# Optimization experiments

Hardware: AMD Instinct MI355X
Metric: run time of the kernel (lower is better)

The kernel has to match this reference:

```python
import jax, jax.numpy as jnp
import numpy as np

K = 10
EPS = 1e-5
SLOPE = 0.01
B, FIN, FOUT, N = 16, 128, 128, 2048


def _bn(x, g, b, axes):
    # training-mode batchnorm over given axes (channel dim is axis 1)
    m = jnp.mean(x, axis=axes, keepdims=True)
    v = jnp.var(x, axis=axes, keepdims=True)
    sh = [1] * x.ndim
    sh[1] = -1
    return (x - m) * jax.lax.rsqrt(v + EPS) * g.reshape(sh) + b.reshape(sh)


def _lrelu(x):
    return jnp.where(x >= 0, x, SLOPE * x)


def _conv1x1(x, W, b):
    return jnp.einsum('bcnk,oc->bonk', x, W) + b[None, :, None, None]


def _forward(x, pc, Wf, bf, gf, betaf, Wx, bx, gx, betax, Wa1, ba1, ga1, beta_a1, Wa2, ba2, ga2, beta_a2, Wi, bi, gi, beta_i, W2, b2, g2, beta2):
    Bsz, Fin, Npts = x.shape
    k = K
    # --- kNN graph build: pairwise sq-dist via bmm, full sort, drop self ---
    sq = jnp.sum(x * x, axis=1)  # [B,N]
    dist = -2.0 * jnp.einsum('bdn,bdm->bnm', x, x) + sq[:, :, None] + sq[:, None, :]
    idx = jnp.argsort(dist, axis=2)[:, :, 1:k + 1]  # [B,N,k]
    gather = jax.vmap(lambda f, i: f[:, i])  # [C,N],[N,k] -> [C,N,k]
    nbr = gather(x, idx)
    nbr_xyz = gather(pc, idx)
    e_fea = jnp.concatenate([jnp.broadcast_to(x[..., None], (Bsz, Fin, Npts, k)), nbr - x[..., None]], axis=1)   # [B,2Fin,N,k]
    e_xyz = jnp.concatenate([jnp.broadcast_to(pc[..., None], (Bsz, 3, Npts, k)), nbr_xyz - pc[..., None]], axis=1)  # [B,6,N,k]
    # --- bilateral attention weights ---
    w = _lrelu(_bn(_conv1x1(e_fea, Wf, bf), gf, betaf, (0, 2, 3))) * _lrelu(_bn(_conv1x1(e_xyz, Wx, bx), gx, betax, (0, 2, 3)))
    w = _lrelu(_bn(_conv1x1(w, Wa1, ba1), ga1, beta_a1, (0, 2, 3)))
    w = _lrelu(_bn(_conv1x1(w, Wa2, ba2), ga2, beta_a2, (0, 2, 3)))
    w = jax.nn.softmax(w, axis=-1)  # [B,2Fin,N,k]
    # --- interpolation conv over neighbour axis (kernel [1, k//2+1]) ---
    inte = jax.lax.conv_general_dilated(e_fea, Wi, (1, 1), 'VALID', dimension_numbers=('NCHW', 'OIHW', 'NCHW')) + bi[None, :, None, None]
    inte = _lrelu(_bn(inte, gi, beta_i, (0, 2, 3)))  # [B,4Fin,N,k-k//2]
    inte = jnp.transpose(inte, (0, 2, 1, 3)).reshape(Bsz, Npts, 2 * Fin, k)  # channel-pair interleave, same layout as torch .view
    inte = jnp.transpose(inte, (0, 2, 1, 3)) * w  # [B,2Fin,N,k]
    merge = jnp.concatenate([e_fea, inte], axis=3)  # [B,2Fin,N,2k]
    # conv2: kernel [1,2k] spans full width -> width-1 output, as einsum
    out = jnp.einsum('bcnw,ocw->bon', merge, W2[:, :, 0, :]) + b2[None, :, None]  # [B,2Fout,N]
    out = jnp.maximum(_bn(out, g2, beta2, (0, 2)), 0.0)
    Fout = out.shape[1] // 2
    return out.reshape(Bsz, Fout, 2 * Npts)


def setup_inputs() -> dict:
    ks = jax.random.split(jax.random.key(0), 10)
    s = 0.05
    return {
        'x': jax.random.normal(ks[0], (B, FIN, N), jnp.float32),
        'pc': jax.random.normal(ks[1], (B, 3, N), jnp.float32),
        'Wf': jax.random.normal(ks[2], (16, 2 * FIN), jnp.float32) * s,
        'bf': jnp.zeros((16,), jnp.float32), 'gf': jnp.ones((16,), jnp.float32), 'betaf': jnp.zeros((16,), jnp.float32),
        'Wx': jax.random.normal(ks[3], (16, 6), jnp.float32) * s,
        'bx': jnp.zeros((16,), jnp.float32), 'gx': jnp.ones((16,), jnp.float32), 'betax': jnp.zeros((16,), jnp.float32),
        'Wa1': jax.random.normal(ks[4], (64, 16), jnp.float32) * s,
        'ba1': jnp.zeros((64,), jnp.float32), 'ga1': jnp.ones((64,), jnp.float32), 'beta_a1': jnp.zeros((64,), jnp.float32),
        'Wa2': jax.random.normal(ks[5], (2 * FIN, 64), jnp.float32) * s,
        'ba2': jnp.zeros((2 * FIN,), jnp.float32), 'ga2': jnp.ones((2 * FIN,), jnp.float32), 'beta_a2': jnp.zeros((2 * FIN,), jnp.float32),
        'Wi': jax.random.normal(ks[6], (4 * FIN, 2 * FIN, 1, K // 2 + 1), jnp.float32) * s,
        'bi': jnp.zeros((4 * FIN,), jnp.float32), 'gi': jnp.ones((4 * FIN,), jnp.float32), 'beta_i': jnp.zeros((4 * FIN,), jnp.float32),
        'W2': jax.random.normal(ks[7], (2 * FOUT, 2 * FIN, 1, 2 * K), jnp.float32) * s,
        'b2': jnp.zeros((2 * FOUT,), jnp.float32), 'g2': jnp.ones((2 * FOUT,), jnp.float32), 'beta2': jnp.zeros((2 * FOUT,), jnp.float32),
    }


def reference(x, pc, Wf, bf, gf, betaf, Wx, bx, gx, betax, Wa1, ba1, ga1, beta_a1, Wa2, ba2, ga2, beta_a2, Wi, bi, gi, beta_i, W2, b2, g2, beta2):
    return _forward(x, pc, Wf, bf, gf, betaf, Wx, bx, gx, betax, Wa1, ba1, ga1, beta_a1, Wa2, ba2, ga2, beta_a2, Wi, bi, gi, beta_i, W2, b2, g2, beta2)
```

## Files before the change

kernel.cpp:

```cpp
#include <hip/hip_runtime.h>
#include <hip/hip_bf16.h>
#include <cstdio>
#include <cstddef>

#define B_    16
#define FIN_  128
#define N_    2048
#define K_    10
#define EPS_  1e-5f
#define SLOPE_ 0.01f

typedef float f32x4 __attribute__((ext_vector_type(4)));
typedef short s16x8 __attribute__((ext_vector_type(8)));
typedef short s16x4 __attribute__((ext_vector_type(4)));

constexpr int SUM_F=0,   SS_F=16,   SUM_X=32,  SS_X=48;
constexpr int SUM_A1=64, SS_A1=128, SUM_A2=192,SS_A2=448;
constexpr int SUM_I=704, SS_I=1216, SUM_O=1728,SS_O=1984;
constexpr int SCALE_F=2240, SHIFT_F=2256, SCALE_X=2272, SHIFT_X=2288;
constexpr int SCALE_A1=2304, SHIFT_A1=2368, SCALE_A2=2432, SHIFT_A2=2688;
constexpr int SCALE_I=2944, SHIFT_I=3456, SCALE_O=3968, SHIFT_O=4224;
constexpr int STATS_TOTAL=4480;
constexpr int AUX_TOTAL = 64 + 4096;

constexpr int KW2_ = 3968;
constexpr int CHUNK_ = 8192;

__device__ __forceinline__ float lrelu(float v){ return v >= 0.f ? v : SLOPE_*v; }
__device__ __forceinline__ float wave_sum(float v){
  #pragma unroll
  for (int o = 32; o > 0; o >>= 1) v += __shfl_down(v, o, 64);
  return v;
}
__device__ __forceinline__ unsigned short f2bf(float f){
  __hip_bfloat16 h = __float2bfloat16(f);
  return *reinterpret_cast<unsigned short*>(&h);
}
__device__ __forceinline__ float bf2f(unsigned short u){
  __hip_bfloat16 h = *reinterpret_cast<__hip_bfloat16*>(&u);
  return __bfloat162float(h);
}

__global__ void k_zero(float* s, float* aux){
  for (int i = threadIdx.x; i < STATS_TOTAL; i += 256) s[i] = 0.f;
  for (int i = threadIdx.x; i < AUX_TOTAL; i += 256) aux[i] = 0.f;
}

__global__ __launch_bounds__(256) void k_xt(const float* __restrict__ x, float* __restrict__ xT){
  __shared__ float t[32][33];
  const int b = blockIdx.z;
  const int c0 = blockIdx.x*32, n0 = blockIdx.y*32;
  const int tx = threadIdx.x & 31, ty = threadIdx.x >> 5;
  #pragma unroll
  for (int s = 0; s < 32; s += 8)
    t[ty+s][tx] = x[((size_t)b*FIN_ + c0+ty+s)*N_ + n0 + tx];
  __syncthreads();
  #pragma unroll
  for (int s = 0; s < 32; s += 8)
    xT[((size_t)b*N_ + n0+ty+s)*FIN_ + c0 + tx] = t[tx][ty+s];
}

__global__ __launch_bounds__(256) void k_sq(const float* __restrict__ x, float* __restrict__ sq){
  int id = blockIdx.x*256 + threadIdx.x;
  int b = id >> 11, n = id & (N_-1);
  const float* xb = x + (size_t)b*FIN_*N_ + n;
  float part[16];
  #pragma unroll
  for (int p = 0; p < 16; ++p){
    float a = 0.f;
    #pragma unroll
    for (int q = 0; q < 8; ++q){
      float v = xb[(size_t)(p + 16*q)*N_];
      a = __fmaf_rn(v, v, a);
    }
    part[p] = a;
  }
  #pragma unroll
  for (int off = 8; off > 0; off >>= 1){
    #pragma unroll
    for (int l = 0; l < off; ++l)
      part[l] = __fadd_rn(part[l], part[l+off]);
  }
  sq[id] = part[0];
}

__global__ __launch_bounds__(256, 2) void k_knn(const float* __restrict__ x, const float* __restrict__ sq,
                                                int* __restrict__ idx){
  __shared__ __align__(16) char smem[61440];
  float* xi = (float*)smem;
  const int b = blockIdx.y, i0 = blockIdx.x*64;
  const float* xb = x + (size_t)b*FIN_*N_;
  for (int t = threadIdx.x; t < FIN_*64; t += 256){
    int c = t >> 6, ii = t & 63;
    xi[t] = xb[(size_t)c*N_ + i0 + ii];
  }
  __syncthreads();
  const int ty = threadIdx.x >> 4;
  const int tx = threadIdx.x & 15;
  const int ibase = ty*4;
  const f32x4 sqi = *(const f32x4*)&sq[b*N_ + i0 + ibase];
  float bd[4][10]; int bi[4][10];
  #pragma unroll
  for (int ii=0;ii<4;++ii)
    #pragma unroll
    for (int s=0;s<10;++s){ bd[ii][s] = 1e30f; bi[ii][s] = -1; }

  for (int j0 = 0; j0 < N_; j0 += 64){
    const int jb = j0 + tx*4;
    const float* xjp = xb + jb;
    f32x4 acc[4] = {};
    #pragma unroll 8
    for (int c = 0; c < FIN_; ++c){
      const f32x4 a  = *(const f32x4*)&xi[c*64 + ibase];
      const f32x4 bb = *(const f32x4*)&xjp[(size_t)c*N_];
      #pragma unroll
      for (int ii=0;ii<4;++ii){
        #pragma unroll
        for (int m=0;m<4;++m)
          acc[ii][m] = __fmaf_rn(a[ii], bb[m], acc[ii][m]);
      }
    }
    const f32x4 sqj = *(const f32x4*)&sq[b*N_ + jb];
    #pragma unroll
    for (int ii=0;ii<4;++ii){
      const int i = i0 + ibase + ii;
      #pragma unroll
      for (int m=0;m<4;++m){
        int j = jb + m;
        float d = __fadd_rn(__fadd_rn(__fmul_rn(-2.f, acc[ii][m]), sqi[ii]), sqj[m]);
        if (j == i) d = 1e30f;
        if (d < bd[ii][9]){
          bd[ii][9] = d; bi[ii][9] = j;
          #pragma unroll
          for (int s = 9; s > 0; --s){
            if (bd[ii][s] < bd[ii][s-1]){
              float td = bd[ii][s]; bd[ii][s] = bd[ii][s-1]; bd[ii][s-1] = td;
              int ti = bi[ii][s]; bi[ii][s] = bi[ii][s-1]; bi[ii][s-1] = ti;
            }
          }
        }
      }
    }
  }

  __syncthreads();
  float* dbuf = (float*)smem;
  unsigned short* ibuf = (unsigned short*)(smem + 40960);
  #pragma unroll
  for (int ii=0;ii<4;++ii)
    #pragma unroll
    for (int s=0;s<10;++s){
      dbuf[(tx*10+s)*64 + ibase+ii] = bd[ii][s];
      ibuf[(tx*10+s)*64 + ibase+ii] = (unsigned short)bi[ii][s];
    }
  __syncthreads();
  if (threadIdx.x < 64){
    const int rr = threadIdx.x;
    int p[16];
    #pragma unroll
    for (int qq=0;qq<16;++qq) p[qq]=0;
    int* op = idx + ((size_t)b*N_ + i0 + rr)*K_;
    for (int s = 0; s < K_; ++s){
      float dm = 1e38f; int im = 0x7fffffff; int qm = 0;
      #pragma unroll
      for (int qq = 0; qq < 16; ++qq){
        int pq = p[qq];
        float d  = (pq < 10) ? dbuf[(qq*10+pq)*64 + rr] : 1e38f;
        int   jd = (pq < 10) ? (int)ibuf[(qq*10+pq)*64 + rr] : 0x7fffffff;
        bool take = (d < dm) || (d == dm && jd < im);
        if (take){ dm = d; im = jd; qm = qq; }
      }
      #pragma unroll
      for (int qq = 0; qq < 16; ++qq) if (qm == qq) p[qq]++;
      op[s] = im;
    }
  }
}

__global__ __launch_bounds__(256) void k_fx_stats(const float* __restrict__ xT, const float* __restrict__ pc,
                                                  const int* __restrict__ idx,
                                                  const float* __restrict__ Wf, const float* __restrict__ Wx,
                                                  float* __restrict__ stats, float* __restrict__ ytmp){
  __shared__ float wfT[256*16];
  __shared__ float wxT[6*16];
  for (int t = threadIdx.x; t < 256*16; t += 256){ int c = t >> 4, o = t & 15; wfT[t] = Wf[o*256 + c]; }
  if (threadIdx.x < 96){ int cc = threadIdx.x >> 4, o = threadIdx.x & 15; wxT[cc*16+o] = Wx[o*6+cc]; }
  __syncthreads();
  const int id = blockIdx.x*256 + threadIdx.x;
  const int b = id >> 11, n = id & (N_-1);
  const float* xs = xT + (size_t)id*FIN_;
  const float* pb = pc + (size_t)b*3*N_;
  float yc[16];
  #pragma unroll
  for (int o=0;o<16;++o) yc[o]=0.f;
  for (int c=0;c<FIN_;c+=4){
    const f32x4 v4 = *(const f32x4*)&xs[c];
    #pragma unroll
    for (int e=0;e<4;++e){
      float v = v4[e];
      #pragma unroll
      for (int o=0;o<16;++o) yc[o] += wfT[(c+e)*16+o]*v;
    }
  }
  float p0=pb[n], p1=pb[N_+n], p2=pb[2*N_+n];
  float sf[16], ssf[16], sx[16], ssx[16];
  #pragma unroll
  for (int o=0;o<16;++o){ sf[o]=0.f;ssf[o]=0.f;sx[o]=0.f;ssx[o]=0.f; }
  for (int kk=0;kk<K_;++kk){
    int j = idx[(size_t)id*K_ + kk];
    const float* xj = xT + ((size_t)b*N_ + j)*FIN_;
    float y[16];
    #pragma unroll
    for (int o=0;o<16;++o) y[o]=yc[o];
    for (int c=0;c<FIN_;c+=4){
      const f32x4 a4 = *(const f32x4*)&xj[c];
      const f32x4 s4 = *(const f32x4*)&xs[c];
      #pragma unroll
      for (int e=0;e<4;++e){
        float d = a4[e]-s4[e];
        #pragma unroll
        for (int o=0;o<16;++o) y[o] += wfT[(128+c+e)*16+o]*d;
      }
    }
    float q0=pb[j]-p0, q1=pb[N_+j]-p1, q2=pb[2*N_+j]-p2;
    float vx[16];
    #pragma unroll
    for (int o=0;o<16;++o){
      vx[o] = wxT[0*16+o]*p0 + wxT[1*16+o]*p1 + wxT[2*16+o]*p2
            + wxT[3*16+o]*q0 + wxT[4*16+o]*q1 + wxT[5*16+o]*q2;
    }
    #pragma unroll
    for (int o=0;o<16;++o){
      sf[o]+=y[o]; ssf[o]+=y[o]*y[o];
      sx[o]+=vx[o]; ssx[o]+=vx[o]*vx[o];
    }
    float* yt = ytmp + ((size_t)id*K_ + kk)*32;
    #pragma unroll
    for (int o=0;o<16;++o){ yt[o] = y[o]; yt[16+o] = vx[o]; }
  }
  #pragma unroll
  for (int o=0;o<16;++o){
    float v;
    v = wave_sum(sf[o]);  if ((threadIdx.x&63)==0) atomicAdd(&stats[SUM_F+o], v);
    v = wave_sum(ssf[o]); if ((threadIdx.x&63)==0) atomicAdd(&stats[SS_F+o], v);
    v = wave_sum(sx[o]);  if ((threadIdx.x&63)==0) atomicAdd(&stats[SUM_X+o], v);
    v = wave_sum(ssx[o]); if ((threadIdx.x&63)==0) atomicAdd(&stats[SS_X+o], v);
  }
}

__global__ void k_finalize(float* stats, int sumoff, int ssoff, int nch, float cnt_inv,
                           const float* __restrict__ g, const float* __restrict__ bt,
                           int scoff, int shoff){
  int c = threadIdx.x;
  if (c < nch){
    float mean = stats[sumoff+c]*cnt_inv;
    float var  = stats[ssoff+c]*cnt_inv - mean*mean;
    float rstd = rsqrtf(var + EPS_);
    float sc = g[c]*rstd;
    stats[scoff+c] = sc;
    stats[shoff+c] = bt[c] - mean*sc;
  }
}

__global__ __launch_bounds__(256) void k_wapply(const float* __restrict__ ytmp, const float* __restrict__ stats,
                                                float* __restrict__ wprod){
  __shared__ float s4[64];
  if (threadIdx.x < 64) s4[threadIdx.x] = stats[SCALE_F + threadIdx.x];
  __syncthreads();
  const int e = blockIdx.x*256 + threadIdx.x;
  const float* yt = ytmp + (size_t)e*32;
  float* wp = wprod + (size_t)e*16;
  #pragma unroll
  for (int o=0;o<16;++o){
    float a  = lrelu(yt[o]*s4[o] + s4[16+o]);
    float bb = lrelu(yt[16+o]*s4[32+o] + s4[48+o]);
    wp[o] = a*bb;
  }
}

__global__ __launch_bounds__(256) void k_a1_stats(const float* __restrict__ wprod, const float* __restrict__ Wa1,
                                                  float* __restrict__ stats){
  __shared__ float wp[64*16];
  const int oc = threadIdx.x & 63, sub = threadIdx.x >> 6;
  float wa[16];
  #pragma unroll
  for (int j = 0; j < 16; ++j) wa[j] = Wa1[oc*16+j];
  float s = 0.f, ss = 0.f;
  for (int tile = blockIdx.x; tile < 5120; tile += gridDim.x){
    __syncthreads();
    for (int t = threadIdx.x; t < 1024; t += 256) wp[t] = wprod[(size_t)tile*1024 + t];
    __syncthreads();
    for (int p = sub*16; p < sub*16+16; ++p){
      float y = 0.f;
      #pragma unroll
      for (int j = 0; j < 16; ++j) y += wa[j]*wp[p*16+j];
      s += y; ss += y*y;
    }
  }
  atomicAdd(&stats[SUM_A1+oc], s);
  atomicAdd(&stats[SS_A1+oc], ss);
}

__global__ __launch_bounds__(256) void k_a2g(const float* __restrict__ wprod, const float* __restrict__ Wa1,
                                             const float* __restrict__ stats, float* __restrict__ aux){
  __shared__ float wp[64*16];
  __shared__ float a1t[64*64];
  __shared__ float wa1T[16*64];
  __shared__ float sc1[64], sh1[64];
  for (int t=threadIdx.x;t<1024;t+=256){ int j=t&63, jj=t>>6; wa1T[jj*64+j] = Wa1[j*16+jj]; }
  if (threadIdx.x < 64){ sc1[threadIdx.x]=stats[SCALE_A1+threadIdx.x]; sh1[threadIdx.x]=stats[SHIFT_A1+threadIdx.x]; }
  const int i  = threadIdx.x >> 2;
  const int jq = threadIdx.x & 3;
  f32x4 g0={0.f,0.f,0.f,0.f}, g1={0.f,0.f,0.f,0.f}, g2={0.f,0.f,0.f,0.f}, g3={0.f,0.f,0.f,0.f};
  float s = 0.f;
  for (int tile = blockIdx.x; tile < 5120; tile += gridDim.x){
    __syncthreads();
    for (int t=threadIdx.x;t<1024;t+=256) wp[t] = wprod[(size_t)tile*1024 + t];
    __syncthreads();
    for (int t=threadIdx.x;t<4096;t+=256){
      int p = t >> 6, j = t & 63;
      float yv=0.f;
      #pragma unroll
      for (int jj=0;jj<16;++jj) yv += wa1T[jj*64+j]*wp[p*16+jj];
      a1t[t] = lrelu(yv*sc1[j]+sh1[j]);
    }
    __syncthreads();
    #pragma unroll 4
    for (int p=0;p<64;++p){
      const float ai = a1t[p*64 + i];
      const f32x4* row = (const f32x4*)&a1t[p*64 + jq*16];
      g0 += ai*row[0]; g1 += ai*row[1]; g2 += ai*row[2]; g3 += ai*row[3];
      if (jq == 0) s += ai;
    }
  }
  float* G = aux + 64;
  const int base = i*64 + jq*16;
  #pragma unroll
  for (int r=0;r<4;++r){ atomicAdd(&G[base+r],    g0[r]); }
  #pragma unroll
  for (int r=0;r<4;++r){ atomicAdd(&G[base+4+r],  g1[r]); }
  #pragma unroll
  for (int r=0;r<4;++r){ atomicAdd(&G[base+8+r],  g2[r]); }
  #pragma unroll
  for (int r=0;r<4;++r){ atomicAdd(&G[base+12+r], g3[r]); }
  if (jq == 0) atomicAdd(&aux[i], s);
}

__global__ void k_a2fin(const float* __restrict__ aux, const float* __restrict__ Wa2,
                        float* __restrict__ stats){
  __shared__ float G[4096];
  __shared__ float S[64];
  for (int t = threadIdx.x; t < 4096; t += 256) G[t] = aux[64 + t];
  if (threadIdx.x < 64) S[threadIdx.x] = aux[threadIdx.x];
  __syncthreads();
  const int oc = threadIdx.x;
  float w[64];
  #pragma unroll
  for (int j=0;j<64;++j) w[j] = Wa2[oc*64+j];
  float sum = 0.f;
  #pragma unroll
  for (int j=0;j<64;++j) sum += w[j]*S[j];
  float ss = 0.f;
  for (int i=0;i<64;++i){
    float gi = 0.f;
    #pragma unroll
    for (int j=0;j<64;++j) gi += w[j]*G[i*64+j];
    ss += w[i]*gi;
  }
  stats[SUM_A2+oc] = sum;
  stats[SS_A2+oc]  = ss;
}

__global__ __launch_bounds__(256) void k_prepAi(const float* __restrict__ Wi, unsigned short* __restrict__ Ai){
  const int total = 512*896;
  for (int e = blockIdx.x*256 + threadIdx.x; e < total; e += gridDim.x*256){
    int o = e / 896, k = e - o*896;
    float v;
    if (k < 768){
      int u = k >> 7, c = k & 127;
      v = Wi[(size_t)o*1536 + (128+c)*6 + u];
    } else {
      const float* p = &Wi[(size_t)o*1536 + (size_t)(k-768)*6];
      v = p[0]+p[1]+p[2]+p[3]+p[4]+p[5];
    }
    Ai[e] = f2bf(v);
  }
}

__global__ __launch_bounds__(256) void k_prepA2(const float* __restrict__ W2,
                                                unsigned short* __restrict__ A2hi,
                                                unsigned short* __restrict__ A2lo){
  const int total = 256*KW2_;
  for (int e = blockIdx.x*256 + threadIdx.x; e < total; e += gridDim.x*256){
    int oc = e / KW2_, k = e - oc*KW2_;
    const float* wr = &W2[(size_t)oc*5120];
    float v;
    if (k < 2560){
      int o = k & 511, t5 = k >> 9;
      int cch = o >> 1, w = (o & 1)*5 + t5;
      v = wr[cch*20 + 10 + w];
    } else if (k < 3840){
      int kk = k - 2560; int w = kk >> 7, c = kk & 127;
      v = wr[(128+c)*20 + w];
    } else {
      int c = k - 3840;
      float s = 0.f;
      #pragma unroll
      for (int w = 0; w < 10; ++w) s += wr[c*20+w] - wr[(128+c)*20+w];
      v = s;
    }
    unsigned short hi = f2bf(v);
    float lo = v - bf2f(hi);
    A2hi[e] = hi;
    A2lo[e] = f2bf(lo);
  }
}

__global__ __launch_bounds__(256) void k_gather(const float* __restrict__ xT, const int* __restrict__ idx,
                                                unsigned short* __restrict__ Bd, int pxbase){
  const int e = blockIdx.x*256 + threadIdx.x;
  const int pxl = e >> 4, sub = e & 15;
  const int px = pxbase + pxl;
  const int c0 = sub*8;
  const float* xs = xT + (size_t)px*FIN_ + c0;
  const f32x4 s0 = *(const f32x4*)&xs[0];
  const f32x4 s1 = *(const f32x4*)&xs[4];
  unsigned short* bo = Bd + (size_t)pxl*1408;
  const size_t bb = (size_t)(px >> 11)*N_*FIN_;
  const int* ip = idx + (size_t)px*K_;
  #pragma unroll
  for (int w = 0; w < 10; ++w){
    int j = ip[w];
    const float* xj = xT + bb + (size_t)j*FIN_ + c0;
    const f32x4 a0 = *(const f32x4*)&xj[0];
    const f32x4 a1 = *(const f32x4*)&xj[4];
    unsigned short tw[8];
    tw[0]=f2bf(a0.x-s0.x); tw[1]=f2bf(a0.y-s0.y); tw[2]=f2bf(a0.z-s0.z); tw[3]=f2bf(a0.w-s0.w);
    tw[4]=f2bf(a1.x-s1.x); tw[5]=f2bf(a1.y-s1.y); tw[6]=f2bf(a1.z-s1.z); tw[7]=f2bf(a1.w-s1.w);
    *(s16x8*)&bo[w*128 + c0] = *(const s16x8*)tw;
  }
  unsigned short tw[8];
  tw[0]=f2bf(s0.x); tw[1]=f2bf(s0.y); tw[2]=f2bf(s0.z); tw[3]=f2bf(s0.w);
  tw[4]=f2bf(s1.x); tw[5]=f2bf(s1.y); tw[6]=f2bf(s1.z); tw[7]=f2bf(s1.w);
  *(s16x8*)&bo[1280 + c0] = *(const s16x8*)tw;
}

__global__ __launch_bounds__(256) void k_gemmI(const unsigned short* __restrict__ Bd,
                                               const unsigned short* __restrict__ Ai,
                                               __hip_bfloat16* __restrict__ ybuf, float* __restrict__ stats,
                                               int pxbase){
  __shared__ __align__(16) unsigned short As[128*72];
  __shared__ __align__(16) unsigned short Bs[128*72];
  const int o0 = blockIdx.x * 128;
  const int c0 = blockIdx.y * 128;
  const int t5 = blockIdx.z;
  const int rowA = threadIdx.x >> 1;
  const int kA   = (threadIdx.x & 1)*32;
  const unsigned short* arow = Ai + (size_t)(o0+rowA)*896 + kA;
  const int colJ = threadIdx.x >> 1;
  const int kB   = (threadIdx.x & 1)*32;
  const unsigned short* brow = Bd + (size_t)(c0 + colJ)*1408;
  const int wave = threadIdx.x >> 6, lane = threadIdx.x & 63;
  const int quad = lane >> 4, l16 = lane & 15;
  const int wm = wave & 1, wn = wave >> 1;

  f32x4 acc[4][4] = {};

  for (int k0 = 0; k0 < 896; k0 += 64){
    __syncthreads();
    {
      unsigned short* dst = &As[rowA*72 + kA];
      *(s16x8*)&dst[0]  = *(const s16x8*)&arow[k0+0];
      *(s16x8*)&dst[8]  = *(const s16x8*)&arow[k0+8];
      *(s16x8*)&dst[16] = *(const s16x8*)&arow[k0+16];
      *(s16x8*)&dst[24] = *(const s16x8*)&arow[k0+24];
    }
    {
      const int kk = k0 + kB;
      const unsigned short* src = brow + ((kk < 768) ? ((t5 + (kk >> 7))*128 + (kk & 127))
                                                     : (1280 + (kk - 768)));
      unsigned short* dst = &Bs[colJ*72 + kB];
      *(s16x8*)&dst[0]  = *(const s16x8*)&src[0];
      *(s16x8*)&dst[8]  = *(const s16x8*)&src[8];
      *(s16x8*)&dst[16] = *(const s16x8*)&src[16];
      *(s16x8*)&dst[24] = *(const s16x8*)&src[24];
    }
    __syncthreads();
    #pragma unroll
    for (int ks = 0; ks < 2; ++ks){
      s16x8 af[4], bfr[4];
      #pragma unroll
      for (int mt = 0; mt < 4; ++mt)
        af[mt] = *(const s16x8*)&As[(wm*64 + mt*16 + l16)*72 + ks*32 + quad*8];
      #pragma unroll
      for (int nt = 0; nt < 4; ++nt)
        bfr[nt] = *(const s16x8*)&Bs[(wn*64 + nt*16 + l16)*72 + ks*32 + quad*8];
      #pragma unroll
      for (int mt = 0; mt < 4; ++mt)
        #pragma unroll
        for (int nt = 0; nt < 4; ++nt)
          acc[mt][nt] = __builtin_amdgcn_mfma_f32_16x16x32_bf16(af[mt], bfr[nt], acc[mt][nt], 0, 0, 0);
    }
  }

  __syncthreads();
  float* red = (float*)As;
  red[threadIdx.x] = 0.f;
  __syncthreads();
  #pragma unroll
  for (int mt = 0; mt < 4; ++mt){
    const int rowLbase = wm*64 + mt*16 + quad*4;
    #pragma unroll
    for (int reg = 0; reg < 4; ++reg){
      float s = 0.f, ss = 0.f;
      #pragma unroll
      for (int nt = 0; nt < 4; ++nt){ float v = acc[mt][nt][reg]; s += v; ss += v*v; }
      atomicAdd(&red[(rowLbase+reg)*2+0], s);
      atomicAdd(&red[(rowLbase+reg)*2+1], ss);
    }
  }
  #pragma unroll
  for (int mt = 0; mt < 4; ++mt){
    #pragma unroll
    for (int nt = 0; nt < 4; ++nt){
      const int px = pxbase + c0 + wn*64 + nt*16 + l16;
      const int ob = wm*64 + mt*16 + quad*4;
      s16x4 w;
      #pragma unroll
      for (int reg = 0; reg < 4; ++reg) w[reg] = (short)f2bf(acc[mt][nt][reg]);
      *(s16x4*)&ybuf[(size_t)px*2560 + t5*512 + o0 + ob] = w;
    }
  }
  __syncthreads();
  if (threadIdx.x < 128){
    atomicAdd(&stats[SUM_I + o0 + threadIdx.x], red[threadIdx.x*2+0]);
    atomicAdd(&stats[SS_I + o0 + threadIdx.x], red[threadIdx.x*2+1]);
  }
}

__global__ __launch_bounds__(256, 4) void k_wchain(const float* __restrict__ wprod, const float* __restrict__ Wa1,
                                                   const float* __restrict__ Wa2, const float* __restrict__ stats,
                                                   __hip_bfloat16* __restrict__ ybuf, int pxPerBlk){
  __shared__ float wp[160];
  __shared__ float a1l[640];
  __shared__ float wa1T[16*64];
  __shared__ float sc1[64], sh1[64];
  for (int t = threadIdx.x; t < 1024; t += 256){ int j = t & 63, jj = t >> 6; wa1T[jj*64+j] = Wa1[j*16+jj]; }
  if (threadIdx.x < 64){ sc1[threadIdx.x]=stats[SCALE_A1+threadIdx.x]; sh1[threadIdx.x]=stats[SHIFT_A1+threadIdx.x]; }
  const int c = threadIdx.x;
  f32x4 wa2v[16];
  #pragma unroll
  for (int j4=0;j4<16;++j4) wa2v[j4] = *(const f32x4*)&Wa2[c*64 + j4*4];
  const float sc2 = stats[SCALE_A2+c], sh2 = stats[SHIFT_A2+c];
  const float sci0 = stats[SCALE_I + 2*c], shi0 = stats[SHIFT_I + 2*c];
  const float sci1 = stats[SCALE_I + 2*c+1], shi1 = stats[SHIFT_I + 2*c+1];

  for (int pp = 0; pp < pxPerBlk; ++pp){
    const size_t px = (size_t)blockIdx.x*pxPerBlk + pp;
    __syncthreads();
    if (threadIdx.x < 160) wp[threadIdx.x] = wprod[px*160 + threadIdx.x];
    __syncthreads();
    for (int t = threadIdx.x; t < 640; t += 256){
      int kk = t >> 6, j = t & 63;
      float y=0.f;
      #pragma unroll
      for (int jj=0;jj<16;++jj) y += wa1T[jj*64+j]*wp[kk*16+jj];
      a1l[kk*64+j] = lrelu(y*sc1[j]+sh1[j]);
    }
    __syncthreads();
    float wt[10];
    #pragma unroll
    for (int kk=0;kk<10;++kk){
      f32x4 acc = {0.f,0.f,0.f,0.f};
      #pragma unroll
      for (int j4=0;j4<16;++j4){
        const f32x4 a = *(const f32x4*)&a1l[kk*64 + j4*4];
        acc += wa2v[j4]*a;
      }
      float y = (acc.x+acc.y)+(acc.z+acc.w);
      wt[kk] = lrelu(y*sc2+sh2);
    }
    float mx = wt[0];
    #pragma unroll
    for (int kk=1;kk<10;++kk) mx = fmaxf(mx, wt[kk]);
    float sum = 0.f;
    #pragma unroll
    for (int kk=0;kk<10;++kk){ wt[kk] = __expf(wt[kk]-mx); sum += wt[kk]; }
    float inv = 1.f/sum;
    __hip_bfloat16* yb = ybuf + px*2560;
    #pragma unroll
    for (int q = 0; q < 10; ++q){
      const int t5q = (q < 5) ? q : q-5;
      const int ii  = t5q*512 + 2*c + ((q < 5) ? 0 : 1);
      float v = __bfloat162float(yb[ii]);
      float sc = (q < 5) ? sci0 : sci1;
      float sh = (q < 5) ? shi0 : shi1;
      yb[ii] = __float2bfloat16(lrelu(v*sc+sh) * (wt[q]*inv));
    }
  }
}

__global__ __launch_bounds__(256) void k_w2(const float* __restrict__ xT, const int* __restrict__ idx,
                                            const __hip_bfloat16* __restrict__ inte,
                                            const unsigned short* __restrict__ A2hi,
                                            const unsigned short* __restrict__ A2lo,
                                            float* __restrict__ outpre, float* __restrict__ stats){
  __shared__ __align__(16) unsigned short AsH[128*40];
  __shared__ __align__(16) unsigned short AsL[128*40];
  __shared__ __align__(16) unsigned short BsH[128*40];
  __shared__ __align__(16) unsigned short BsL[128*40];
  __shared__ int sIdx[128*10];
  const int r0 = blockIdx.x * 128;
  const int c0 = blockIdx.y * 128;
  for (int t = threadIdx.x; t < 1280; t += 256) sIdx[t] = idx[(size_t)c0*10 + t];
  const int rowA  = threadIdx.x >> 1;
  const int halfA = threadIdx.x & 1;
  const unsigned short* ahrow = A2hi + (size_t)(r0+rowA)*KW2_ + halfA*16;
  const unsigned short* alrow = A2lo + (size_t)(r0+rowA)*KW2_ + halfA*16;
  const int colJ  = threadIdx.x >> 1;
  const int cHalf = (threadIdx.x & 1)*16;
  const int pxJ   = c0 + colJ;
  const size_t selfJ  = (size_t)pxJ*FIN_;
  const size_t bbaseJ = (size_t)(pxJ >> 11)*N_*FIN_;
  const __hip_bfloat16* ibJ = inte + (size_t)pxJ*2560;
  const int wave = threadIdx.x >> 6, lane = threadIdx.x & 63;
  const int quad = lane >> 4, l16 = lane & 15;
  const int wm = wave & 1, wn = wave >> 1;

  f32x4 acc[4][4] = {};

  for (int k0 = 0; k0 < KW2_; k0 += 32){
    __syncthreads();
    {
      *(s16x8*)&AsH[rowA*40 + halfA*16]     = *(const s16x8*)&ahrow[k0];
      *(s16x8*)&AsH[rowA*40 + halfA*16 + 8] = *(const s16x8*)&ahrow[k0+8];
      *(s16x8*)&AsL[rowA*40 + halfA*16]     = *(const s16x8*)&alrow[k0];
      *(s16x8*)&AsL[rowA*40 + halfA*16 + 8] = *(const s16x8*)&alrow[k0+8];
    }
    if (k0 < 2560){
      *(s16x8*)&BsH[colJ*40 + cHalf]     = *(const s16x8*)(ibJ + k0 + cHalf);
      *(s16x8*)&BsH[colJ*40 + cHalf + 8] = *(const s16x8*)(ibJ + k0 + cHalf + 8);
    } else {
      const float* src;
      if (k0 < 3840){
        const int w  = (k0 - 2560) >> 7;
        const int cb = ((k0 - 2560) & 127) + cHalf;
        const int j  = sIdx[colJ*10 + w];
        src = &xT[bbaseJ + (size_t)j*FIN_ + cb];
      } else {
        src = &xT[selfJ + (k0 - 3840) + cHalf];
      }
      unsigned short th[16], tl[16];
      #pragma unroll
      for (int q = 0; q < 4; ++q){
        const f32x4 v = *(const f32x4*)&src[q*4];
        #pragma unroll
        for (int e2 = 0; e2 < 4; ++e2){
          float f = v[e2];
          unsigned short h = f2bf(f);
          float r = f - bf2f(h);
          th[q*4+e2] = h;
          tl[q*4+e2] = f2bf(r);
        }
      }
      *(s16x8*)&BsH[colJ*40 + cHalf]     = *(const s16x8*)&th[0];
      *(s16x8*)&BsH[colJ*40 + cHalf + 8] = *(const s16x8*)&th[8];
      *(s16x8*)&BsL[colJ*40 + cHalf]     = *(const s16x8*)&tl[0];
      *(s16x8*)&BsL[colJ*40 + cHalf + 8] = *(const s16x8*)&tl[8];
    }
    __syncthreads();
    s16x8 ah[4], al[4], bh[4];
    #pragma unroll
    for (int mt = 0; mt < 4; ++mt){
      ah[mt] = *(const s16x8*)&AsH[(wm*64 + mt*16 + l16)*40 + quad*8];
      al[mt] = *(const s16x8*)&AsL[(wm*64 + mt*16 + l16)*40 + quad*8];
    }
    #pragma unroll
    for (int nt = 0; nt < 4; ++nt)
      bh[nt] = *(const s16x8*)&BsH[(wn*64 + nt*16 + l16)*40 + quad*8];
    #pragma unroll
    for (int mt = 0; mt < 4; ++mt)
      #pragma unroll
      for (int nt = 0; nt < 4; ++nt){
        acc[mt][nt] = __builtin_amdgcn_mfma_f32_16x16x32_bf16(ah[mt], bh[nt], acc[mt][nt], 0, 0, 0);
        acc[mt][nt] = __builtin_amdgcn_mfma_f32_16x16x32_bf16(al[mt], bh[nt], acc[mt][nt], 0, 0, 0);
      }
    if (k0 >= 2560){
      s16x8 bl[4];
      #pragma unroll
      for (int nt = 0; nt < 4; ++nt)
        bl[nt] = *(const s16x8*)&BsL[(wn*64 + nt*16 + l16)*40 + quad*8];
      #pragma unroll
      for (int mt = 0; mt < 4; ++mt)
        #pragma unroll
        for (int nt = 0; nt < 4; ++nt)
          acc[mt][nt] = __builtin_amdgcn_mfma_f32_16x16x32_bf16(ah[mt], bl[nt], acc[mt][nt], 0, 0, 0);
    }
  }

  __syncthreads();
  float* red = (float*)AsH;
  red[threadIdx.x] = 0.f;
  __syncthreads();
  #pragma unroll
  for (int mt = 0; mt < 4; ++mt){
    const int rowLbase = wm*64 + mt*16 + quad*4;
    #pragma unroll
    for (int reg = 0; reg < 4; ++reg){
      float s = 0.f, ss = 0.f;
      #pragma unroll
      for (int nt = 0; nt < 4; ++nt){ float v = acc[mt][nt][reg]; s += v; ss += v*v; }
      atomicAdd(&red[(rowLbase+reg)*2+0], s);
      atomicAdd(&red[(rowLbase+reg)*2+1], ss);
    }
  }
  #pragma unroll
  for (int mt = 0; mt < 4; ++mt){
    #pragma unroll
    for (int nt = 0; nt < 4; ++nt){
      const int col = c0 + wn*64 + nt*16 + l16;
      const int rowb = r0 + wm*64 + mt*16 + quad*4;
      #pragma unroll
      for (int reg = 0; reg < 4; ++reg)
        outpre[(size_t)(rowb+reg)*32768 + col] = acc[mt][nt][reg];
    }
  }
  __syncthreads();
  if (threadIdx.x < 128){
    atomicAdd(&stats[SUM_O + r0 + threadIdx.x], red[threadIdx.x*2+0]);
    atomicAdd(&stats[SS_O + r0 + threadIdx.x], red[threadIdx.x*2+1]);
  }
}

__global__ __launch_bounds__(256) void k_final(const float* __restrict__ outpre, const float* __restrict__ stats,
                                               float* __restrict__ out){
  const unsigned total = (unsigned)B_*128u*4096u;
  for (unsigned e = blockIdx.x*256u + threadIdx.x; e < total; e += gridDim.x*256u){
    unsigned b = e >> 19;
    unsigned rem = e & ((1u<<19)-1u);
    unsigned f = rem >> 12;
    unsigned m = rem & 4095u;
    unsigned half = m >> 11;
    unsigned n = m & 2047u;
    unsigned c = f*2u + half;
    float pre = outpre[(size_t)c*32768 + b*2048 + n];
    float v = pre*stats[SCALE_O+c] + stats[SHIFT_O+c];
    out[e] = fmaxf(v, 0.f);
  }
}

extern "C" void kernel_launch(void* const* d_in, const int* in_sizes, int n_in,
                              void* d_out, int out_size, void* d_ws, size_t ws_size,
                              hipStream_t stream) {
  (void)in_sizes; (void)n_in; (void)out_size;
  const float* x    = (const float*)d_in[0];
  const float* pc   = (const float*)d_in[1];
  const float* Wf   = (const float*)d_in[2];
  const float* gf   = (const float*)d_in[4];
  const float* btf  = (const float*)d_in[5];
  const float* Wx   = (const float*)d_in[6];
  const float* gx   = (const float*)d_in[8];
  const float* btx  = (const float*)d_in[9];
  const float* Wa1  = (const float*)d_in[10];
  const float* ga1  = (const float*)d_in[12];
  const float* bta1 = (const float*)d_in[13];
  const float* Wa2  = (const float*)d_in[14];
  const float* ga2  = (const float*)d_in[16];
  const float* bta2 = (const float*)d_in[17];
  const float* Wi   = (const float*)d_in[18];
  const float* gi   = (const float*)d_in[20];
  const float* bti  = (const float*)d_in[21];
  const float* W2   = (const float*)d_in[22];
  const float* g2   = (const float*)d_in[24];
  const float* bt2  = (const float*)d_in[25];
  float* out = (float*)d_out;

  char* ws = (char*)d_ws;
  float*  stats  = (float*)ws;
  int*    idx    = (int*)  (ws + 32768);
  float*  sq     = (float*)(ws + 1343488);
  float*  aux    = (float*)(ws + 1474560);
  float*  wprod  = (float*)(ws + 1605632);
  float*  xT     = (float*)(ws + 22577152);
  unsigned short* A2hi = (unsigned short*)(ws + 39354368);
  unsigned short* A2lo = (unsigned short*)(ws + 41385984);
  float*  outpre = (float*)(ws + 44597248);
  unsigned short* Ai = (unsigned short*)(ws + 44597248);
  unsigned short* Bd = (unsigned short*)(ws + 45645824);
  __hip_bfloat16* ybuf = (__hip_bfloat16*)(ws + 78151680);
  float* ytmp = (float*)(ws + 78151680);
  if (ws_size < 245923840ULL) {
    fprintf(stderr, "kernel_launch: ws_size %zu < required 245923840\n", ws_size);
    return;
  }

  k_zero<<<1, 256, 0, stream>>>(stats, aux);
  k_xt<<<dim3(FIN_/32, N_/32, B_), 256, 0, stream>>>(x, xT);
  k_sq<<<(B_*N_)/256, 256, 0, stream>>>(x, sq);
  k_knn<<<dim3(N_/64, B_), 256, 0, stream>>>(x, sq, idx);
  k_prepAi<<<1024, 256, 0, stream>>>(Wi, Ai);
  k_prepA2<<<1024, 256, 0, stream>>>(W2, A2hi, A2lo);

  k_fx_stats<<<(B_*N_)/256, 256, 0, stream>>>(xT, pc, idx, Wf, Wx, stats, ytmp);
  k_finalize<<<1, 512, 0, stream>>>(stats, SUM_F, SS_F, 16, 1.f/327680.f, gf, btf, SCALE_F, SHIFT_F);
  k_finalize<<<1, 512, 0, stream>>>(stats, SUM_X, SS_X, 16, 1.f/327680.f, gx, btx, SCALE_X, SHIFT_X);

  k_wapply<<<1280, 256, 0, stream>>>(ytmp, stats, wprod);
  k_a1_stats<<<512, 256, 0, stream>>>(wprod, Wa1, stats);
  k_finalize<<<1, 512, 0, stream>>>(stats, SUM_A1, SS_A1, 64, 1.f/327680.f, ga1, bta1, SCALE_A1, SHIFT_A1);

  k_a2g<<<512, 256, 0, stream>>>(wprod, Wa1, stats, aux);
  k_a2fin<<<1, 256, 0, stream>>>(aux, Wa2, stats);
  k_finalize<<<1, 512, 0, stream>>>(stats, SUM_A2, SS_A2, 256, 1.f/327680.f, ga2, bta2, SCALE_A2, SHIFT_A2);

  for (int ch = 0; ch < (B_*N_)/CHUNK_; ++ch){
    k_gather<<<(CHUNK_*16)/256, 256, 0, stream>>>(xT, idx, Bd, ch*CHUNK_);
    k_gemmI<<<dim3(4, CHUNK_/128, 5), 256, 0, stream>>>(Bd, Ai, ybuf, stats, ch*CHUNK_);
  }
  k_finalize<<<1, 512, 0, stream>>>(stats, SUM_I, SS_I, 512, 1.f/163840.f, gi, bti, SCALE_I, SHIFT_I);

  k_wchain<<<2048, 256, 0, stream>>>(wprod, Wa1, Wa2, stats, ybuf, (B_*N_)/2048);

  k_w2<<<dim3(2, 256), 256, 0, stream>>>(xT, idx, ybuf, A2hi, A2lo, outpre, stats);
  k_finalize<<<1, 512, 0, stream>>>(stats, SUM_O, SS_O, 256, 1.f/32768.f, g2, bt2, SCALE_O, SHIFT_O);

  k_final<<<4096, 256, 0, stream>>>(outpre, stats, out);
}
```

Baseline: 2.289 ms.

## Precompute per-point projections so edge conv becomes gather-add instead of per-neighbor GEMV

```diff
diff --git a/kernel.cpp b/kernel.cpp
--- a/kernel.cpp
+++ b/kernel.cpp
@@ -177,30 +177,47 @@
   }
 }
 
-__global__ __launch_bounds__(256) void k_fx_stats(const float* __restrict__ xT, const float* __restrict__ pc,
-                                                  const int* __restrict__ idx,
-                                                  const float* __restrict__ Wf, const float* __restrict__ Wx,
+__global__ __launch_bounds__(256) void k_prepZ(const float* __restrict__ xT, const float* __restrict__ Wf,
+                                               float* __restrict__ zbuf){
+  __shared__ float wfT[256*16];
+  for (int t = threadIdx.x; t < 256*16; t += 256){ int c = t >> 4, o = t & 15; wfT[t] = Wf[o*256 + c]; }
+  __syncthreads();
+  const int id = blockIdx.x*256 + threadIdx.x;
+  const float* xs = xT + (size_t)id*FIN_;
+  float yc[16], z[16];
+  #pragma unroll
+  for (int o=0;o<16;++o){ yc[o]=0.f; z[o]=0.f; }
+  for (int c=0;c<FIN_;c+=4){
+    const f32x4 v4 = *(const f32x4*)&xs[c];
+    #pragma unroll
+    for (int e=0;e<4;++e){
+      float v = v4[e];
+      #pragma unroll
+      for (int o=0;o<16;++o){
+        yc[o] += wfT[(c+e)*16+o]*v;
+        z[o]  += wfT[(128+c+e)*16+o]*v;
+      }
+    }
+  }
+  float* zb = zbuf + (size_t)id*32;
+  #pragma unroll
+  for (int o=0;o<16;++o){ zb[o] = yc[o] - z[o]; zb[16+o] = z[o]; }
+}
+
+__global__ __launch_bounds__(256) void k_fx_stats(const float* __restrict__ zbuf, const float* __restrict__ pc,
+                                                  const int* __restrict__ idx, const float* __restrict__ Wx,
                                                   float* __restrict__ stats, float* __restrict__ ytmp){
-  __shared__ float wfT[256*16];
   __shared__ float wxT[6*16];
-  for (int t = threadIdx.x; t < 256*16; t += 256){ int c = t >> 4, o = t & 15; wfT[t] = Wf[o*256 + c]; }
   if (threadIdx.x < 96){ int cc = threadIdx.x >> 4, o = threadIdx.x & 15; wxT[cc*16+o] = Wx[o*6+cc]; }
   __syncthreads();
   const int id = blockIdx.x*256 + threadIdx.x;
   const int b = id >> 11, n = id & (N_-1);
-  const float* xs = xT + (size_t)id*FIN_;
   const float* pb = pc + (size_t)b*3*N_;
-  float yc[16];
-  #pragma unroll
-  for (int o=0;o<16;++o) yc[o]=0.f;
-  for (int c=0;c<FIN_;c+=4){
-    const f32x4 v4 = *(const f32x4*)&xs[c];
-    #pragma unroll
-    for (int e=0;e<4;++e){
-      float v = v4[e];
-      #pragma unroll
-      for (int o=0;o<16;++o) yc[o] += wfT[(c+e)*16+o]*v;
-    }
+  float base[16];
+  {
+    const float* zb = zbuf + (size_t)id*32;
+    #pragma unroll
+    for (int o=0;o<16;++o) base[o] = zb[o];
   }
   float p0=pb[n], p1=pb[N_+n], p2=pb[2*N_+n];
   float sf[16], ssf[16], sx[16], ssx[16];
@@ -208,19 +225,12 @@
   for (int o=0;o<16;++o){ sf[o]=0.f;ssf[o]=0.f;sx[o]=0.f;ssx[o]=0.f; }
   for (int kk=0;kk<K_;++kk){
     int j = idx[(size_t)id*K_ + kk];
-    const float* xj = xT + ((size_t)b*N_ + j)*FIN_;
+    const float* zj = zbuf + ((size_t)(b*N_ + j))*32 + 16;
     float y[16];
     #pragma unroll
-    for (int o=0;o<16;++o) y[o]=yc[o];
-    for (int c=0;c<FIN_;c+=4){
-      const f32x4 a4 = *(const f32x4*)&xj[c];
-      const f32x4 s4 = *(const f32x4*)&xs[c];
-      #pragma unroll
-      for (int e=0;e<4;++e){
-        float d = a4[e]-s4[e];
-        #pragma unroll
-        for (int o=0;o<16;++o) y[o] += wfT[(128+c+e)*16+o]*d;
-      }
+    for (int o=0;o<16;o+=4){
+      const f32x4 zv = *(const f32x4*)&zj[o];
+      y[o+0]=base[o+0]+zv.x; y[o+1]=base[o+1]+zv.y; y[o+2]=base[o+2]+zv.z; y[o+3]=base[o+3]+zv.w;
     }
     float q0=pb[j]-p0, q1=pb[N_+j]-p1, q2=pb[2*N_+j]-p2;
     float vx[16];
@@ -781,6 +791,7 @@
   float*  sq     = (float*)(ws + 1343488);
   float*  aux    = (float*)(ws + 1474560);
   float*  wprod  = (float*)(ws + 1605632);
+  float*  zbuf   = (float*)(ws + 1605632);
   float*  xT     = (float*)(ws + 22577152);
   unsigned short* A2hi = (unsigned short*)(ws + 39354368);
   unsigned short* A2lo = (unsigned short*)(ws + 41385984);
@@ -798,10 +809,11 @@
   k_xt<<<dim3(FIN_/32, N_/32, B_), 256, 0, stream>>>(x, xT);
   k_sq<<<(B_*N_)/256, 256, 0, stream>>>(x, sq);
   k_knn<<<dim3(N_/64, B_), 256, 0, stream>>>(x, sq, idx);
+  k_prepZ<<<(B_*N_)/256, 256, 0, stream>>>(xT, Wf, zbuf);
   k_prepAi<<<1024, 256, 0, stream>>>(Wi, Ai);
   k_prepA2<<<1024, 256, 0, stream>>>(W2, A2hi, A2lo);
 
-  k_fx_stats<<<(B_*N_)/256, 256, 0, stream>>>(xT, pc, idx, Wf, Wx, stats, ytmp);
+  k_fx_stats<<<(B_*N_)/256, 256, 0, stream>>>(zbuf, pc, idx, Wx, stats, ytmp);
   k_finalize<<<1, 512, 0, stream>>>(stats, SUM_F, SS_F, 16, 1.f/327680.f, gf, btf, SCALE_F, SHIFT_F);
   k_finalize<<<1, 512, 0, stream>>>(stats, SUM_X, SS_X, 16, 1.f/327680.f, gx, btx, SCALE_X, SHIFT_X);
 
```

After: 2.207 ms. -3.6%, faster.
